# Optimization experiments

Hardware: AMD Instinct MI355X
Metric: run time of the kernel (lower is better)

Reference implementation:

```python
import jax, jax.numpy as jnp
import numpy as np

HOPS = 3  # C[i].weight tied to A[i+1].weight -> HOPS+1 distinct tables E_0..E_HOPS


def setup_inputs() -> dict:
    key = jax.random.key(0)
    ks = jax.random.split(key, 10)
    B, M, K, E, G, V = 32, 2048, 4, 128, 128, 50000
    s = 1.0 / np.sqrt(E).astype(np.float32)
    context = jax.random.randint(ks[0], (B, M, K), 0, V)          # memory (triples)
    h_ = jax.random.normal(ks[1], (B, G), dtype=jnp.float32)      # prev GRU hidden
    y_ = jax.random.randint(ks[2], (B,), 0, V)                    # prev token
    emb = jax.random.normal(ks[3], (HOPS + 1, V, E), dtype=jnp.float32) * 0.1
    W_ih = jax.random.normal(ks[4], (3 * G, E), dtype=jnp.float32) * s
    W_hh = jax.random.normal(ks[5], (3 * G, G), dtype=jnp.float32) * s
    b_ih = jax.random.normal(ks[6], (3 * G,), dtype=jnp.float32) * s
    b_hh = jax.random.normal(ks[7], (3 * G,), dtype=jnp.float32) * s
    W_vocab = jax.random.normal(ks[8], (V, 2 * E), dtype=jnp.float32) * s
    b_vocab = jax.random.normal(ks[9], (V,), dtype=jnp.float32) * s
    return dict(context=context, h_=h_, y_=y_, emb=emb, W_ih=W_ih, W_hh=W_hh,
                b_ih=b_ih, b_hh=b_hh, W_vocab=W_vocab, b_vocab=b_vocab)


def gru_cell(x, h, W_ih, W_hh, b_ih, b_hh):
    # PyTorch GRU cell semantics (r, z, n gate order).
    gi = x @ W_ih.T + b_ih
    gh = h @ W_hh.T + b_hh
    i_r, i_z, i_n = jnp.split(gi, 3, axis=-1)
    h_r, h_z, h_n = jnp.split(gh, 3, axis=-1)
    r = jax.nn.sigmoid(i_r + h_r)
    z = jax.nn.sigmoid(i_z + h_z)
    n = jnp.tanh(i_n + r * h_n)
    return (1.0 - z) * n + z * h


def reference(context, h_, y_, emb, W_ih, W_hh, b_ih, b_hh, W_vocab, b_vocab):
    x = emb[0][y_]                                   # [B, E] A[0] embed of prev token
    h = gru_cell(x, h_, W_ih, W_hh, b_ih, b_hh)      # [B, G], G == E
    q = h
    o1 = None
    attn = None
    for hop in range(HOPS):
        mA = emb[hop][context].sum(axis=2)           # gather [B,M,K,E] -> sum over K -> [B,M,E]
        p = jnp.einsum('bme,be->bm', mA, q)          # attention scores over memory slots
        attn = jax.nn.softmax(p, axis=1)             # [B, M]
        mC = emb[hop + 1][context].sum(axis=2)       # C[hop] table (tied to A[hop+1])
        o = jnp.einsum('bm,bme->be', attn, mC)       # memory read [B, E]
        q = q + o
        if hop == 0:
            o1 = o
    logits = jnp.concatenate([h, o1], axis=1) @ W_vocab.T + b_vocab  # [B, V]
    p_vocab = jax.nn.softmax(logits, axis=1)
    return h, p_vocab, attn
```

## Files before the change

### kernel.cpp

```cpp
#include <hip/hip_runtime.h>
#include <math.h>

#define BB 32
#define MM 2048
#define KK 4
#define EE 128
#define GG 128
#define VV 50000
#define HOPS 3

__global__ __launch_bounds__(384) void gru_kernel(
    const float* __restrict__ emb0,
    const int*   __restrict__ y,
    const float* __restrict__ hprev,
    const float* __restrict__ W_ih,
    const float* __restrict__ W_hh,
    const float* __restrict__ b_ih,
    const float* __restrict__ b_hh,
    float* __restrict__ h_out,
    float* __restrict__ q)
{
    int b = blockIdx.x;
    int t = threadIdx.x;
    __shared__ float x[EE], h[GG], gi[3*GG], gh[3*GG];
    if (t < EE)            x[t]       = emb0[(size_t)y[b]*EE + t];
    else if (t < 2*EE)     h[t-EE]    = hprev[b*GG + (t-EE)];
    __syncthreads();
    {
        float accI = b_ih[t], accH = b_hh[t];
        const float* wi = W_ih + (size_t)t*EE;
        const float* wh = W_hh + (size_t)t*GG;
        #pragma unroll 8
        for (int e = 0; e < EE; e++) { accI += x[e]*wi[e]; accH += h[e]*wh[e]; }
        gi[t] = accI; gh[t] = accH;
    }
    __syncthreads();
    if (t < GG) {
        float r = 1.f/(1.f + __expf(-(gi[t]        + gh[t])));
        float z = 1.f/(1.f + __expf(-(gi[GG+t]     + gh[GG+t])));
        float n = tanhf(gi[2*GG+t] + r*gh[2*GG+t]);
        float hn = (1.f - z)*n + z*h[t];
        h_out[b*GG + t] = hn;
        q[b*GG + t]     = hn;
    }
}

__global__ __launch_bounds__(256) void scores_kernel(
    const float* __restrict__ embT,
    const int*   __restrict__ ctx,
    const float* __restrict__ q,
    float* __restrict__ p)
{
    int gid  = blockIdx.x * 4 + (threadIdx.x >> 6);
    int lane = threadIdx.x & 63;
    int b    = gid >> 11;
    const int4 c = *(const int4*)(ctx + (size_t)gid*KK);
    float2 qv = *(const float2*)(q + b*EE + lane*2);
    float2 v0 = *(const float2*)(embT + (size_t)c.x*EE + lane*2);
    float2 v1 = *(const float2*)(embT + (size_t)c.y*EE + lane*2);
    float2 v2 = *(const float2*)(embT + (size_t)c.z*EE + lane*2);
    float2 v3 = *(const float2*)(embT + (size_t)c.w*EE + lane*2);
    float sx = v0.x + v1.x + v2.x + v3.x;
    float sy = v0.y + v1.y + v2.y + v3.y;
    float acc = sx*qv.x + sy*qv.y;
    #pragma unroll
    for (int off = 32; off; off >>= 1) acc += __shfl_down(acc, off);
    if (lane == 0) p[gid] = acc;
}

__global__ __launch_bounds__(256) void softmax_m_kernel(
    const float* __restrict__ p,
    float* __restrict__ attn)
{
    int b = blockIdx.x, t = threadIdx.x;
    const float* row = p + (size_t)b*MM;
    float v[8];
    float mx = -INFINITY;
    #pragma unroll
    for (int i = 0; i < 8; i++) { v[i] = row[t + i*256]; mx = fmaxf(mx, v[i]); }
    __shared__ float red[6];
    int w = t >> 6, lane = t & 63;
    #pragma unroll
    for (int off = 32; off; off >>= 1) mx = fmaxf(mx, __shfl_down(mx, off));
    if (lane == 0) red[w] = mx;
    __syncthreads();
    if (t == 0) { float m2 = fmaxf(fmaxf(red[0],red[1]), fmaxf(red[2],red[3])); red[4] = m2; }
    __syncthreads();
    mx = red[4];
    float sum = 0.f;
    #pragma unroll
    for (int i = 0; i < 8; i++) { v[i] = __expf(v[i] - mx); sum += v[i]; }
    #pragma unroll
    for (int off = 32; off; off >>= 1) sum += __shfl_down(sum, off);
    if (lane == 0) red[w] = sum;
    __syncthreads();
    if (t == 0) { red[5] = 1.f / (red[0]+red[1]+red[2]+red[3]); }
    __syncthreads();
    float rs = red[5];
    #pragma unroll
    for (int i = 0; i < 8; i++) attn[(size_t)b*MM + t + i*256] = v[i]*rs;
}

__global__ __launch_bounds__(256) void oacc_kernel(
    const float* __restrict__ embT,
    const int*   __restrict__ ctx,
    const float* __restrict__ attn,
    float* __restrict__ o_part)
{
    int blk = blockIdx.x;
    int b = blk >> 5, s = blk & 31;
    int w = threadIdx.x >> 6, lane = threadIdx.x & 63;
    int m0 = s*64 + w*16;
    float ax = 0.f, ay = 0.f;
    for (int i = 0; i < 16; i++) {
        int m = m0 + i;
        float a = attn[(size_t)b*MM + m];
        const int4 c = *(const int4*)(ctx + (size_t)(b*MM + m)*KK);
        float2 v0 = *(const float2*)(embT + (size_t)c.x*EE + lane*2);
        float2 v1 = *(const float2*)(embT + (size_t)c.y*EE + lane*2);
        float2 v2 = *(const float2*)(embT + (size_t)c.z*EE + lane*2);
        float2 v3 = *(const float2*)(embT + (size_t)c.w*EE + lane*2);
        ax += a * (v0.x + v1.x + v2.x + v3.x);
        ay += a * (v0.y + v1.y + v2.y + v3.y);
    }
    __shared__ float red[4][EE];
    red[w][lane*2]   = ax;
    red[w][lane*2+1] = ay;
    __syncthreads();
    if (threadIdx.x < EE) {
        int e = threadIdx.x;
        float v = red[0][e] + red[1][e] + red[2][e] + red[3][e];
        o_part[((size_t)s*BB + b)*EE + e] = v;
    }
}

__global__ __launch_bounds__(256) void qupd_kernel(
    const float* __restrict__ o_part,
    float* __restrict__ q,
    float* __restrict__ o1,
    int save_o1)
{
    int i = blockIdx.x*256 + threadIdx.x;
    float v = 0.f;
    #pragma unroll 8
    for (int s = 0; s < 32; s++) v += o_part[(size_t)s*BB*EE + i];
    q[i] += v;
    if (save_o1) o1[i] = v;
}

__global__ __launch_bounds__(256) void logits_kernel(
    const float* __restrict__ h,
    const float* __restrict__ o1,
    const float* __restrict__ Wv,
    const float* __restrict__ bv,
    float* __restrict__ logits)
{
    __shared__ float Ut[256][32];
    __shared__ float Wt[32][132];
    int t = threadIdx.x;
    for (int i = t; i < 256*32; i += 256) {
        int e = i >> 5, b = i & 31;
        Ut[e][b] = (e < GG) ? h[b*GG + e] : o1[b*EE + (e - GG)];
    }
    int vg = t & 31;
    int bg = t >> 5;
    int v0 = blockIdx.x * 128;
    float acc[4][4];
    #pragma unroll
    for (int i = 0; i < 4; i++)
        #pragma unroll
        for (int j = 0; j < 4; j++) acc[i][j] = 0.f;

    int vrow = t >> 1;
    int half = t & 1;
    const float* wrow = Wv + (size_t)(v0 + vrow)*256 + half*16;
    bool vok = (v0 + vrow) < VV;

    for (int ec = 0; ec < 256; ec += 32) {
        __syncthreads();
        #pragma unroll
        for (int j = 0; j < 4; j++) {
            float4 w = make_float4(0.f, 0.f, 0.f, 0.f);
            if (vok) w = *(const float4*)(wrow + ec + j*4);
            int e0 = half*16 + j*4;
            Wt[e0+0][vrow] = w.x;
            Wt[e0+1][vrow] = w.y;
            Wt[e0+2][vrow] = w.z;
            Wt[e0+3][vrow] = w.w;
        }
        __syncthreads();
        #pragma unroll 8
        for (int e = 0; e < 32; e++) {
            float4 w = *(const float4*)(&Wt[e][vg*4]);
            float4 u = *(const float4*)(&Ut[ec + e][bg*4]);
            acc[0][0] += w.x*u.x; acc[0][1] += w.x*u.y; acc[0][2] += w.x*u.z; acc[0][3] += w.x*u.w;
            acc[1][0] += w.y*u.x; acc[1][1] += w.y*u.y; acc[1][2] += w.y*u.z; acc[1][3] += w.y*u.w;
            acc[2][0] += w.z*u.x; acc[2][1] += w.z*u.y; acc[2][2] += w.z*u.z; acc[2][3] += w.z*u.w;
            acc[3][0] += w.w*u.x; acc[3][1] += w.w*u.y; acc[3][2] += w.w*u.z; acc[3][3] += w.w*u.w;
        }
    }
    #pragma unroll
    for (int i = 0; i < 4; i++) {
        int v = v0 + vg*4 + i;
        if (v < VV) {
            float bb = bv[v];
            #pragma unroll
            for (int j = 0; j < 4; j++)
                logits[(size_t)(bg*4 + j)*VV + v] = acc[i][j] + bb;
        }
    }
}

#define VCHUNK 6250
__global__ __launch_bounds__(256) void vpart_kernel(
    const float* __restrict__ logits,
    float* __restrict__ part)
{
    int blk = blockIdx.x;
    int b = blk >> 3, c = blk & 7;
    int t = threadIdx.x;
    const float* row = logits + (size_t)b*VV;
    int start = c*VCHUNK;
    int end   = min(start + VCHUNK, VV);
    __shared__ float red[4];
    int w = t >> 6, lane = t & 63;
    float mx = -INFINITY;
    for (int i = start + t; i < end; i += 256) mx = fmaxf(mx, row[i]);
    #pragma unroll
    for (int off = 32; off; off >>= 1) mx = fmaxf(mx, __shfl_down(mx, off));
    if (lane == 0) red[w] = mx;
    __syncthreads();
    float m = fmaxf(fmaxf(red[0], red[1]), fmaxf(red[2], red[3]));
    float sum = 0.f;
    for (int i = start + t; i < end; i += 256) sum += __expf(row[i] - m);
    #pragma unroll
    for (int off = 32; off; off >>= 1) sum += __shfl_down(sum, off);
    __syncthreads();
    if (lane == 0) red[w] = sum;
    __syncthreads();
    if (t == 0) {
        part[blk*2]   = m;
        part[blk*2+1] = red[0] + red[1] + red[2] + red[3];
    }
}

__global__ __launch_bounds__(256) void vfinal_kernel(
    float* __restrict__ logits,
    const float* __restrict__ part)
{
    int i = blockIdx.x*256 + threadIdx.x;
    if (i >= BB*VV) return;
    int b = i / VV;
    const float* pp = part + b*16;
    float M = -INFINITY;
    #pragma unroll
    for (int c = 0; c < 8; c++) M = fmaxf(M, pp[c*2]);
    float S = 0.f;
    #pragma unroll
    for (int c = 0; c < 8; c++) S += pp[c*2+1] * __expf(pp[c*2] - M);
    logits[i] = __expf(logits[i] - M) * (1.f / S);
}

extern "C" void kernel_launch(void* const* d_in, const int* in_sizes, int n_in,
                              void* d_out, int out_size, void* d_ws, size_t ws_size,
                              hipStream_t stream) {
    const int*   ctx    = (const int*)  d_in[0];
    const float* h_prev = (const float*)d_in[1];
    const int*   y      = (const int*)  d_in[2];
    const float* emb    = (const float*)d_in[3];
    const float* W_ih   = (const float*)d_in[4];
    const float* W_hh   = (const float*)d_in[5];
    const float* b_ih   = (const float*)d_in[6];
    const float* b_hh   = (const float*)d_in[7];
    const float* Wv     = (const float*)d_in[8];
    const float* bv     = (const float*)d_in[9];

    float* out_h    = (float*)d_out;
    float* out_pv   = out_h + BB*GG;
    float* out_attn = out_pv + (size_t)BB*VV;

    float* ws     = (float*)d_ws;
    float* q      = ws;
    float* o1     = q + BB*EE;
    float* o_part = o1 + BB*EE;
    float* p      = o_part + 32*BB*EE;
    float* attn   = p + BB*MM;
    float* part   = attn + BB*MM;

    gru_kernel<<<BB, 384, 0, stream>>>(emb, y, h_prev, W_ih, W_hh, b_ih, b_hh, out_h, q);

    for (int hop = 0; hop < HOPS; hop++) {
        const float* embA = emb + (size_t)hop*VV*EE;
        const float* embC = emb + (size_t)(hop+1)*VV*EE;
        scores_kernel<<<(BB*MM)/4, 256, 0, stream>>>(embA, ctx, q, p);
        float* attn_dst = (hop == HOPS-1) ? out_attn : attn;
        softmax_m_kernel<<<BB, 256, 0, stream>>>(p, attn_dst);
        oacc_kernel<<<BB*32, 256, 0, stream>>>(embC, ctx, attn_dst, o_part);
        qupd_kernel<<<(BB*EE)/256, 256, 0, stream>>>(o_part, q, o1, hop == 0 ? 1 : 0);
    }

    logits_kernel<<<(VV + 127)/128, 256, 0, stream>>>(out_h, o1, Wv, bv, out_pv);
    vpart_kernel<<<BB*8, 256, 0, stream>>>(out_pv, part);
    vfinal_kernel<<<(BB*VV + 255)/256, 256, 0, stream>>>(out_pv, part);
}
```

Baseline: 360.5 us.

## Replace per-slot embedding gathers with vocab-space dense GEMMs and scatter-add

Attention scores are computed as d = E_hop·q over the whole vocabulary using a tiled GEMM, then gathered per memory slot by summing four scalar lookups. The memory read scatters attention weights into a per-batch vocabulary histogram with atomics and multiplies it by the next embedding table in a dense tiled kernel. The final hop skips the unused read. This trades random gathers of 128-float rows for streaming the full 50000x128 tables per hop, plus atomics and larger workspaces, and it changes the floating-point summation order.

```diff
diff --git a/kernel.cpp b/kernel.cpp
--- a/kernel.cpp
+++ b/kernel.cpp
@@ -45,46 +45,89 @@
     }
 }
 
-__global__ __launch_bounds__(256) void scores_kernel(
-    const float* __restrict__ embT,
+__global__ __launch_bounds__(256) void dvec_kernel(
+    const float* __restrict__ q,
+    const float* __restrict__ W,
+    float* __restrict__ d)
+{
+    __shared__ float Ut[128][32];
+    __shared__ float Wt[32][132];
+    int t = threadIdx.x;
+    for (int i = t; i < 128*32; i += 256) {
+        int e = i >> 5, b = i & 31;
+        Ut[e][b] = q[b*EE + e];
+    }
+    int vg = t & 31;
+    int bg = t >> 5;
+    int v0 = blockIdx.x * 128;
+    float acc[4][4];
+    #pragma unroll
+    for (int i = 0; i < 4; i++)
+        #pragma unroll
+        for (int j = 0; j < 4; j++) acc[i][j] = 0.f;
+
+    int vrow = t >> 1;
+    int half = t & 1;
+    const float* wrow = W + (size_t)(v0 + vrow)*128 + half*16;
+    bool vok = (v0 + vrow) < VV;
+
+    for (int ec = 0; ec < 128; ec += 32) {
+        __syncthreads();
+        #pragma unroll
+        for (int j = 0; j < 4; j++) {
+            float4 w = make_float4(0.f, 0.f, 0.f, 0.f);
+            if (vok) w = *(const float4*)(wrow + ec + j*4);
+            int e0 = half*16 + j*4;
+            Wt[e0+0][vrow] = w.x;
+            Wt[e0+1][vrow] = w.y;
+            Wt[e0+2][vrow] = w.z;
+            Wt[e0+3][vrow] = w.w;
+        }
+        __syncthreads();
+        #pragma unroll 8
+        for (int e = 0; e < 32; e++) {
+            float4 w = *(const float4*)(&Wt[e][vg*4]);
+            float4 u = *(const float4*)(&Ut[ec + e][bg*4]);
+            acc[0][0] += w.x*u.x; acc[0][1] += w.x*u.y; acc[0][2] += w.x*u.z; acc[0][3] += w.x*u.w;
+            acc[1][0] += w.y*u.x; acc[1][1] += w.y*u.y; acc[1][2] += w.y*u.z; acc[1][3] += w.y*u.w;
+            acc[2][0] += w.z*u.x; acc[2][1] += w.z*u.y; acc[2][2] += w.z*u.z; acc[2][3] += w.z*u.w;
+            acc[3][0] += w.w*u.x; acc[3][1] += w.w*u.y; acc[3][2] += w.w*u.z; acc[3][3] += w.w*u.w;
+        }
+    }
+    #pragma unroll
+    for (int i = 0; i < 4; i++) {
+        int v = v0 + vg*4 + i;
+        if (v < VV) {
+            #pragma unroll
+            for (int j = 0; j < 4; j++)
+                d[(size_t)(bg*4 + j)*VV + v] = acc[i][j];
+        }
+    }
+}
+
+__global__ __launch_bounds__(256) void attn_kernel(
+    const float* __restrict__ d,
     const int*   __restrict__ ctx,
-    const float* __restrict__ q,
-    float* __restrict__ p)
-{
-    int gid  = blockIdx.x * 4 + (threadIdx.x >> 6);
-    int lane = threadIdx.x & 63;
-    int b    = gid >> 11;
-    const int4 c = *(const int4*)(ctx + (size_t)gid*KK);
-    float2 qv = *(const float2*)(q + b*EE + lane*2);
-    float2 v0 = *(const float2*)(embT + (size_t)c.x*EE + lane*2);
-    float2 v1 = *(const float2*)(embT + (size_t)c.y*EE + lane*2);
-    float2 v2 = *(const float2*)(embT + (size_t)c.z*EE + lane*2);
-    float2 v3 = *(const float2*)(embT + (size_t)c.w*EE + lane*2);
-    float sx = v0.x + v1.x + v2.x + v3.x;
-    float sy = v0.y + v1.y + v2.y + v3.y;
-    float acc = sx*qv.x + sy*qv.y;
-    #pragma unroll
-    for (int off = 32; off; off >>= 1) acc += __shfl_down(acc, off);
-    if (lane == 0) p[gid] = acc;
-}
-
-__global__ __launch_bounds__(256) void softmax_m_kernel(
-    const float* __restrict__ p,
     float* __restrict__ attn)
 {
     int b = blockIdx.x, t = threadIdx.x;
-    const float* row = p + (size_t)b*MM;
+    const float* db = d + (size_t)b*VV;
     float v[8];
     float mx = -INFINITY;
     #pragma unroll
-    for (int i = 0; i < 8; i++) { v[i] = row[t + i*256]; mx = fmaxf(mx, v[i]); }
+    for (int i = 0; i < 8; i++) {
+        int m = t + i*256;
+        const int4 c = *(const int4*)(ctx + (size_t)(b*MM + m)*KK);
+        v[i] = db[c.x] + db[c.y] + db[c.z] + db[c.w];
+        mx = fmaxf(mx, v[i]);
+    }
     __shared__ float red[6];
     int w = t >> 6, lane = t & 63;
     #pragma unroll
     for (int off = 32; off; off >>= 1) mx = fmaxf(mx, __shfl_down(mx, off));
     if (lane == 0) red[w] = mx;
     __syncthreads();
-    if (t == 0) { float m2 = fmaxf(fmaxf(red[0],red[1]), fmaxf(red[2],red[3])); red[4] = m2; }
+    if (t == 0) { red[4] = fmaxf(fmaxf(red[0],red[1]), fmaxf(red[2],red[3])); }
     __syncthreads();
     mx = red[4];
     float sum = 0.f;
@@ -101,36 +144,81 @@
     for (int i = 0; i < 8; i++) attn[(size_t)b*MM + t + i*256] = v[i]*rs;
 }
 
-__global__ __launch_bounds__(256) void oacc_kernel(
-    const float* __restrict__ embT,
+__global__ __launch_bounds__(256) void zero_kernel(float* __restrict__ w, int n4)
+{
+    int i = blockIdx.x*256 + threadIdx.x;
+    if (i < n4) ((float4*)w)[i] = make_float4(0.f,0.f,0.f,0.f);
+}
+
+__global__ __launch_bounds__(256) void scatter_kernel(
+    const float* __restrict__ attn,
     const int*   __restrict__ ctx,
-    const float* __restrict__ attn,
+    float* __restrict__ w)
+{
+    int gid = blockIdx.x*256 + threadIdx.x;
+    float a = attn[gid];
+    int b = gid >> 11;
+    const int4 c = *(const int4*)(ctx + (size_t)gid*KK);
+    float* wb = w + (size_t)b*VV;
+    atomicAdd(&wb[c.x], a);
+    atomicAdd(&wb[c.y], a);
+    atomicAdd(&wb[c.z], a);
+    atomicAdd(&wb[c.w], a);
+}
+
+#define OCH 196
+__global__ __launch_bounds__(256) void oaccv_kernel(
+    const float* __restrict__ emb,
+    const float* __restrict__ w,
     float* __restrict__ o_part)
 {
-    int blk = blockIdx.x;
-    int b = blk >> 5, s = blk & 31;
-    int w = threadIdx.x >> 6, lane = threadIdx.x & 63;
-    int m0 = s*64 + w*16;
-    float ax = 0.f, ay = 0.f;
-    for (int i = 0; i < 16; i++) {
-        int m = m0 + i;
-        float a = attn[(size_t)b*MM + m];
-        const int4 c = *(const int4*)(ctx + (size_t)(b*MM + m)*KK);
-        float2 v0 = *(const float2*)(embT + (size_t)c.x*EE + lane*2);
-        float2 v1 = *(const float2*)(embT + (size_t)c.y*EE + lane*2);
-        float2 v2 = *(const float2*)(embT + (size_t)c.z*EE + lane*2);
-        float2 v3 = *(const float2*)(embT + (size_t)c.w*EE + lane*2);
-        ax += a * (v0.x + v1.x + v2.x + v3.x);
-        ay += a * (v0.y + v1.y + v2.y + v3.y);
-    }
-    __shared__ float red[4][EE];
-    red[w][lane*2]   = ax;
-    red[w][lane*2+1] = ay;
-    __syncthreads();
-    if (threadIdx.x < EE) {
-        int e = threadIdx.x;
-        float v = red[0][e] + red[1][e] + red[2][e] + red[3][e];
-        o_part[((size_t)s*BB + b)*EE + e] = v;
+    __shared__ float embS[64][128];
+    __shared__ float wS[64][32];
+    int t = threadIdx.x;
+    int bg = t >> 6;
+    int eg = t & 63;
+    int v0 = blockIdx.x * OCH;
+    int vend = min(v0 + OCH, VV);
+    float acc[8][2];
+    #pragma unroll
+    for (int j = 0; j < 8; j++) { acc[j][0] = 0.f; acc[j][1] = 0.f; }
+
+    for (int vs = v0; vs < vend; vs += 64) {
+        int nv = vend - vs; if (nv > 64) nv = 64;
+        __syncthreads();
+        for (int i = t; i < 64*32; i += 256) {
+            int row = i >> 5, c4 = i & 31;
+            float4 val = make_float4(0.f,0.f,0.f,0.f);
+            if (row < nv) val = *(const float4*)(emb + (size_t)(vs+row)*128 + c4*4);
+            *(float4*)(&embS[row][c4*4]) = val;
+        }
+        for (int i = t; i < 512; i += 256) {
+            int b = i >> 4, vv = (i & 15)*4;
+            float4 val = make_float4(0.f,0.f,0.f,0.f);
+            if (vv < nv) val = *(const float4*)(w + (size_t)b*VV + vs + vv);
+            wS[vv+0][b] = val.x; wS[vv+1][b] = val.y;
+            wS[vv+2][b] = val.z; wS[vv+3][b] = val.w;
+        }
+        __syncthreads();
+        for (int vv = 0; vv < nv; vv++) {
+            float2 ev = *(const float2*)(&embS[vv][eg*2]);
+            float4 w0 = *(const float4*)(&wS[vv][bg*8]);
+            float4 w1 = *(const float4*)(&wS[vv][bg*8+4]);
+            acc[0][0] += w0.x*ev.x; acc[0][1] += w0.x*ev.y;
+            acc[1][0] += w0.y*ev.x; acc[1][1] += w0.y*ev.y;
+            acc[2][0] += w0.z*ev.x; acc[2][1] += w0.z*ev.y;
+            acc[3][0] += w0.w*ev.x; acc[3][1] += w0.w*ev.y;
+            acc[4][0] += w1.x*ev.x; acc[4][1] += w1.x*ev.y;
+            acc[5][0] += w1.y*ev.x; acc[5][1] += w1.y*ev.y;
+            acc[6][0] += w1.z*ev.x; acc[6][1] += w1.z*ev.y;
+            acc[7][0] += w1.w*ev.x; acc[7][1] += w1.w*ev.y;
+        }
+    }
+    float* op = o_part + (size_t)blockIdx.x*BB*EE;
+    #pragma unroll
+    for (int j = 0; j < 8; j++) {
+        op[(bg*8+j)*EE + eg*2]     = acc[j][0];
+        op[(bg*8+j)*EE + eg*2 + 1] = acc[j][1];
     }
 }
 
@@ -143,7 +231,7 @@
     int i = blockIdx.x*256 + threadIdx.x;
     float v = 0.f;
     #pragma unroll 8
-    for (int s = 0; s < 32; s++) v += o_part[(size_t)s*BB*EE + i];
+    for (int s = 0; s < 256; s++) v += o_part[(size_t)s*BB*EE + i];
     q[i] += v;
     if (save_o1) o1[i] = v;
 }
@@ -282,20 +370,27 @@
     float* ws     = (float*)d_ws;
     float* q      = ws;
     float* o1     = q + BB*EE;
-    float* o_part = o1 + BB*EE;
-    float* p      = o_part + 32*BB*EE;
-    float* attn   = p + BB*MM;
+    float* d      = o1 + BB*EE;
+    float* w      = d + (size_t)BB*VV;
+    float* o_part = w + (size_t)BB*VV;
+    float* attn   = o_part + 256*BB*EE;
     float* part   = attn + BB*MM;
+
+    const int dvec_grid = (VV + 127)/128;
+    const int w4 = (BB*VV)/4;
 
     gru_kernel<<<BB, 384, 0, stream>>>(emb, y, h_prev, W_ih, W_hh, b_ih, b_hh, out_h, q);
 
     for (int hop = 0; hop < HOPS; hop++) {
         const float* embA = emb + (size_t)hop*VV*EE;
+        dvec_kernel<<<dvec_grid, 256, 0, stream>>>(q, embA, d);
+        float* attn_dst = (hop == HOPS-1) ? out_attn : attn;
+        attn_kernel<<<BB, 256, 0, stream>>>(d, ctx, attn_dst);
+        if (hop == HOPS-1) break;
         const float* embC = emb + (size_t)(hop+1)*VV*EE;
-        scores_kernel<<<(BB*MM)/4, 256, 0, stream>>>(embA, ctx, q, p);
-        float* attn_dst = (hop == HOPS-1) ? out_attn : attn;
-        softmax_m_kernel<<<BB, 256, 0, stream>>>(p, attn_dst);
-        oacc_kernel<<<BB*32, 256, 0, stream>>>(embC, ctx, attn_dst, o_part);
+        zero_kernel<<<(w4 + 255)/256, 256, 0, stream>>>(w, w4);
+        scatter_kernel<<<(BB*MM)/256, 256, 0, stream>>>(attn_dst, ctx, w);
+        oaccv_kernel<<<256, 256, 0, stream>>>(embC, w, o_part);
         qupd_kernel<<<(BB*EE)/256, 256, 0, stream>>>(o_part, q, o1, hop == 0 ? 1 : 0);
     }
 
```

After: 423.9 us. 17.6% more time.

## Replace memory gathers with dense table-vector products and scattered attention weights

Applied to the files above, without the earlier changes.

The per-slot embedding gathers are replaced by linear algebra. Scores become a dense product of each embedding table with the query (d = E·q over all V), followed by a cheap scalar gather of d at the context indices. The memory read scatters the attention weights into a per-vocab weight vector with atomics and then does a dense streaming product with the C table. This turns random 512-byte row gathers into coalesced full-table streams, which means reading whole 25 MB tables several times per call. It also adds float atomics, which make the summation order nondeterministic. The logits GEMM is also retiled.

```diff
diff --git a/kernel.cpp b/kernel.cpp
--- a/kernel.cpp
+++ b/kernel.cpp
@@ -9,220 +9,266 @@
 #define VV 50000
 #define HOPS 3
 
-__global__ __launch_bounds__(384) void gru_kernel(
-    const float* __restrict__ emb0,
-    const int*   __restrict__ y,
+__global__ __launch_bounds__(256) void gru_zero_kernel(
+    const float* __restrict__ emb0, const int* __restrict__ y,
     const float* __restrict__ hprev,
-    const float* __restrict__ W_ih,
-    const float* __restrict__ W_hh,
-    const float* __restrict__ b_ih,
-    const float* __restrict__ b_hh,
-    float* __restrict__ h_out,
-    float* __restrict__ q)
-{
-    int b = blockIdx.x;
+    const float* __restrict__ W_ih, const float* __restrict__ W_hh,
+    const float* __restrict__ b_ih, const float* __restrict__ b_hh,
+    float* __restrict__ h_out, float* __restrict__ q0,
+    float* __restrict__ wz)
+{
+    int blk = blockIdx.x, t = threadIdx.x;
+    if (blk < BB) {
+        int b = blk;
+        __shared__ float x[EE], hh[GG], gi[3*GG], gh[3*GG];
+        if (t < EE)          x[t]     = emb0[(size_t)y[b]*EE + t];
+        else if (t < 2*EE)   hh[t-EE] = hprev[b*GG + (t-EE)];
+        __syncthreads();
+        for (int g = t; g < 3*GG; g += 256) {
+            float accI = b_ih[g], accH = b_hh[g];
+            const float* wi = W_ih + (size_t)g*EE;
+            const float* wh = W_hh + (size_t)g*GG;
+            #pragma unroll 8
+            for (int e = 0; e < EE; e++) { accI += x[e]*wi[e]; accH += hh[e]*wh[e]; }
+            gi[g] = accI; gh[g] = accH;
+        }
+        __syncthreads();
+        if (t < GG) {
+            float r = 1.f/(1.f + __expf(-(gi[t]      + gh[t])));
+            float z = 1.f/(1.f + __expf(-(gi[GG+t]   + gh[GG+t])));
+            float n = tanhf(gi[2*GG+t] + r*gh[2*GG+t]);
+            float hn = (1.f - z)*n + z*hh[t];
+            h_out[b*GG + t] = hn;
+            q0[b*GG + t]    = hn;
+        }
+    } else {
+        const int total4 = (2*BB*VV)/4;
+        float4* wp = (float4*)wz;
+        for (int i = (blk-BB)*256 + t; i < total4; i += 256*256)
+            wp[i] = make_float4(0.f,0.f,0.f,0.f);
+    }
+}
+
+__global__ __launch_bounds__(256) void dvec_kernel(
+    const float* __restrict__ q0, const float* __restrict__ oa0,
+    const float* __restrict__ oa1, int hop,
+    const float* __restrict__ W, float* __restrict__ d)
+{
+    __shared__ float q2[4096];
     int t = threadIdx.x;
-    __shared__ float x[EE], h[GG], gi[3*GG], gh[3*GG];
-    if (t < EE)            x[t]       = emb0[(size_t)y[b]*EE + t];
-    else if (t < 2*EE)     h[t-EE]    = hprev[b*GG + (t-EE)];
-    __syncthreads();
-    {
-        float accI = b_ih[t], accH = b_hh[t];
-        const float* wi = W_ih + (size_t)t*EE;
-        const float* wh = W_hh + (size_t)t*GG;
-        #pragma unroll 8
-        for (int e = 0; e < EE; e++) { accI += x[e]*wi[e]; accH += h[e]*wh[e]; }
-        gi[t] = accI; gh[t] = accH;
-    }
-    __syncthreads();
-    if (t < GG) {
-        float r = 1.f/(1.f + __expf(-(gi[t]        + gh[t])));
-        float z = 1.f/(1.f + __expf(-(gi[GG+t]     + gh[GG+t])));
-        float n = tanhf(gi[2*GG+t] + r*gh[2*GG+t]);
-        float hn = (1.f - z)*n + z*h[t];
-        h_out[b*GG + t] = hn;
-        q[b*GG + t]     = hn;
-    }
-}
-
-__global__ __launch_bounds__(256) void scores_kernel(
-    const float* __restrict__ embT,
-    const int*   __restrict__ ctx,
-    const float* __restrict__ q,
+    for (int i = t; i < 4096; i += 256) {
+        int e = i >> 5, b = i & 31;
+        float v = q0[b*EE + e];
+        if (hop >= 1) v += oa0[b*EE + e];
+        if (hop >= 2) v += oa1[b*EE + e];
+        q2[(e >> 2)*128 + b*4 + (e & 3)] = v;
+    }
+    __syncthreads();
+    int lane = t & 63, bg = t >> 6;
+    int v = blockIdx.x*64 + lane;
+    const float4* row = (const float4*)(W + (size_t)(v < VV ? v : VV-1)*EE);
+    float acc[8];
+    #pragma unroll
+    for (int k = 0; k < 8; k++) acc[k] = 0.f;
+    #pragma unroll 4
+    for (int c = 0; c < 32; c++) {
+        float4 wv = row[c];
+        const float4* uq = (const float4*)(q2 + c*128 + bg*32);
+        #pragma unroll
+        for (int k = 0; k < 8; k++) {
+            float4 u = uq[k];
+            acc[k] += wv.x*u.x + wv.y*u.y + wv.z*u.z + wv.w*u.w;
+        }
+    }
+    if (v < VV) {
+        #pragma unroll
+        for (int k = 0; k < 8; k++)
+            d[(size_t)(bg*8 + k)*VV + v] = acc[k];
+    }
+}
+
+__global__ __launch_bounds__(256) void pgather_kernel(
+    const float* __restrict__ d, const int* __restrict__ ctx,
     float* __restrict__ p)
 {
-    int gid  = blockIdx.x * 4 + (threadIdx.x >> 6);
-    int lane = threadIdx.x & 63;
-    int b    = gid >> 11;
+    int gid = blockIdx.x*256 + threadIdx.x;
+    int b = gid >> 11;
     const int4 c = *(const int4*)(ctx + (size_t)gid*KK);
-    float2 qv = *(const float2*)(q + b*EE + lane*2);
-    float2 v0 = *(const float2*)(embT + (size_t)c.x*EE + lane*2);
-    float2 v1 = *(const float2*)(embT + (size_t)c.y*EE + lane*2);
-    float2 v2 = *(const float2*)(embT + (size_t)c.z*EE + lane*2);
-    float2 v3 = *(const float2*)(embT + (size_t)c.w*EE + lane*2);
-    float sx = v0.x + v1.x + v2.x + v3.x;
-    float sy = v0.y + v1.y + v2.y + v3.y;
-    float acc = sx*qv.x + sy*qv.y;
-    #pragma unroll
-    for (int off = 32; off; off >>= 1) acc += __shfl_down(acc, off);
-    if (lane == 0) p[gid] = acc;
-}
-
-__global__ __launch_bounds__(256) void softmax_m_kernel(
-    const float* __restrict__ p,
-    float* __restrict__ attn)
+    const float* db = d + (size_t)b*VV;
+    p[gid] = db[c.x] + db[c.y] + db[c.z] + db[c.w];
+}
+
+__global__ __launch_bounds__(256) void softmax_sc_kernel(
+    const float* __restrict__ p, const int* __restrict__ ctx,
+    float* __restrict__ w,
+    float* __restrict__ out_attn,
+    int mode)
 {
     int b = blockIdx.x, t = threadIdx.x;
     const float* row = p + (size_t)b*MM;
-    float v[8];
+    float pv[8];
     float mx = -INFINITY;
     #pragma unroll
-    for (int i = 0; i < 8; i++) { v[i] = row[t + i*256]; mx = fmaxf(mx, v[i]); }
-    __shared__ float red[6];
-    int w = t >> 6, lane = t & 63;
+    for (int i = 0; i < 8; i++) { pv[i] = row[t + i*256]; mx = fmaxf(mx, pv[i]); }
+    __shared__ float red[16];
+    int wv = t >> 6, lane = t & 63;
     #pragma unroll
     for (int off = 32; off; off >>= 1) mx = fmaxf(mx, __shfl_down(mx, off));
-    if (lane == 0) red[w] = mx;
-    __syncthreads();
-    if (t == 0) { float m2 = fmaxf(fmaxf(red[0],red[1]), fmaxf(red[2],red[3])); red[4] = m2; }
+    if (lane == 0) red[wv] = mx;
+    __syncthreads();
+    if (t == 0) red[4] = fmaxf(fmaxf(red[0],red[1]), fmaxf(red[2],red[3]));
     __syncthreads();
     mx = red[4];
     float sum = 0.f;
     #pragma unroll
-    for (int i = 0; i < 8; i++) { v[i] = __expf(v[i] - mx); sum += v[i]; }
+    for (int i = 0; i < 8; i++) { pv[i] = __expf(pv[i] - mx); sum += pv[i]; }
     #pragma unroll
     for (int off = 32; off; off >>= 1) sum += __shfl_down(sum, off);
-    if (lane == 0) red[w] = sum;
-    __syncthreads();
-    if (t == 0) { red[5] = 1.f / (red[0]+red[1]+red[2]+red[3]); }
-    __syncthreads();
-    float rs = red[5];
-    #pragma unroll
-    for (int i = 0; i < 8; i++) attn[(size_t)b*MM + t + i*256] = v[i]*rs;
-}
-
-__global__ __launch_bounds__(256) void oacc_kernel(
-    const float* __restrict__ embT,
-    const int*   __restrict__ ctx,
-    const float* __restrict__ attn,
+    if (lane == 0) red[8 + wv] = sum;
+    __syncthreads();
+    if (t == 0) red[13] = 1.f / (red[8]+red[9]+red[10]+red[11]);
+    __syncthreads();
+    float rs = red[13];
+    if (mode) {
+        #pragma unroll
+        for (int i = 0; i < 8; i++)
+            out_attn[b*MM + t + i*256] = pv[i]*rs;
+    } else {
+        float* wb = w + (size_t)b*VV;
+        const int4* cb = (const int4*)ctx + b*MM;
+        #pragma unroll
+        for (int i = 0; i < 8; i++) {
+            float av = pv[i]*rs;
+            int4 c = cb[t + i*256];
+            atomicAdd(wb + c.x, av);
+            atomicAdd(wb + c.y, av);
+            atomicAdd(wb + c.z, av);
+            atomicAdd(wb + c.w, av);
+        }
+    }
+}
+
+#define OCH 98
+__global__ __launch_bounds__(256) void oaccv_kernel(
+    const float* __restrict__ emb, const float* __restrict__ w,
     float* __restrict__ o_part)
 {
-    int blk = blockIdx.x;
-    int b = blk >> 5, s = blk & 31;
-    int w = threadIdx.x >> 6, lane = threadIdx.x & 63;
-    int m0 = s*64 + w*16;
-    float ax = 0.f, ay = 0.f;
-    for (int i = 0; i < 16; i++) {
-        int m = m0 + i;
-        float a = attn[(size_t)b*MM + m];
-        const int4 c = *(const int4*)(ctx + (size_t)(b*MM + m)*KK);
-        float2 v0 = *(const float2*)(embT + (size_t)c.x*EE + lane*2);
-        float2 v1 = *(const float2*)(embT + (size_t)c.y*EE + lane*2);
-        float2 v2 = *(const float2*)(embT + (size_t)c.z*EE + lane*2);
-        float2 v3 = *(const float2*)(embT + (size_t)c.w*EE + lane*2);
-        ax += a * (v0.x + v1.x + v2.x + v3.x);
-        ay += a * (v0.y + v1.y + v2.y + v3.y);
-    }
-    __shared__ float red[4][EE];
-    red[w][lane*2]   = ax;
-    red[w][lane*2+1] = ay;
-    __syncthreads();
-    if (threadIdx.x < EE) {
-        int e = threadIdx.x;
-        float v = red[0][e] + red[1][e] + red[2][e] + red[3][e];
-        o_part[((size_t)s*BB + b)*EE + e] = v;
+    __shared__ float embS[64*128];
+    __shared__ float wS[64*32];
+    int t = threadIdx.x;
+    int bg = t >> 6, lane = t & 63;
+    int v0 = blockIdx.x * OCH;
+    int vend = min(v0 + OCH, VV);
+    float acc[8][2];
+    #pragma unroll
+    for (int j = 0; j < 8; j++) { acc[j][0] = 0.f; acc[j][1] = 0.f; }
+
+    for (int vs = v0; vs < vend; vs += 64) {
+        int nv = vend - vs; if (nv > 64) nv = 64;
+        __syncthreads();
+        for (int i = t; i < 64*32; i += 256) {
+            int rowi = i >> 5, c4 = i & 31;
+            float4 val = make_float4(0.f,0.f,0.f,0.f);
+            if (rowi < nv) val = *(const float4*)(emb + (size_t)(vs+rowi)*EE + c4*4);
+            *(float4*)(embS + rowi*128 + c4*4) = val;
+        }
+        for (int i = t; i < 512; i += 256) {
+            int b = i >> 4, vv4 = (i & 15)*4;
+            float4 val = make_float4(0.f,0.f,0.f,0.f);
+            if (vv4 < nv) val = *(const float4*)(w + (size_t)b*VV + vs + vv4);
+            wS[(vv4+0)*32 + b] = val.x;
+            wS[(vv4+1)*32 + b] = val.y;
+            wS[(vv4+2)*32 + b] = val.z;
+            wS[(vv4+3)*32 + b] = val.w;
+        }
+        __syncthreads();
+        for (int vv = 0; vv < nv; vv++) {
+            float2 ev  = *(const float2*)(embS + vv*128 + lane*2);
+            float4 w0v = *(const float4*)(wS + vv*32 + bg*8);
+            float4 w1v = *(const float4*)(wS + vv*32 + bg*8 + 4);
+            acc[0][0] += w0v.x*ev.x; acc[0][1] += w0v.x*ev.y;
+            acc[1][0] += w0v.y*ev.x; acc[1][1] += w0v.y*ev.y;
+            acc[2][0] += w0v.z*ev.x; acc[2][1] += w0v.z*ev.y;
+            acc[3][0] += w0v.w*ev.x; acc[3][1] += w0v.w*ev.y;
+            acc[4][0] += w1v.x*ev.x; acc[4][1] += w1v.x*ev.y;
+            acc[5][0] += w1v.y*ev.x; acc[5][1] += w1v.y*ev.y;
+            acc[6][0] += w1v.z*ev.x; acc[6][1] += w1v.z*ev.y;
+            acc[7][0] += w1v.w*ev.x; acc[7][1] += w1v.w*ev.y;
+        }
+    }
+    float* op = o_part + (size_t)blockIdx.x*BB*EE;
+    #pragma unroll
+    for (int j = 0; j < 8; j++) {
+        float2 r; r.x = acc[j][0]; r.y = acc[j][1];
+        *(float2*)(op + (bg*8+j)*EE + lane*2) = r;
     }
 }
 
 __global__ __launch_bounds__(256) void qupd_kernel(
     const float* __restrict__ o_part,
-    float* __restrict__ q,
-    float* __restrict__ o1,
-    int save_o1)
-{
-    int i = blockIdx.x*256 + threadIdx.x;
+    float* __restrict__ o_acc)
+{
+    int i0 = blockIdx.x * 64;
+    int sq = threadIdx.x >> 6;
+    int il = threadIdx.x & 63;
     float v = 0.f;
-    #pragma unroll 8
-    for (int s = 0; s < 32; s++) v += o_part[(size_t)s*BB*EE + i];
-    q[i] += v;
-    if (save_o1) o1[i] = v;
+    for (int s = sq; s < 512; s += 4)
+        v += o_part[(size_t)s*BB*EE + i0 + il];
+    __shared__ float red[4][64];
+    red[sq][il] = v;
+    __syncthreads();
+    if (threadIdx.x < 64)
+        o_acc[i0 + threadIdx.x] = red[0][threadIdx.x] + red[1][threadIdx.x]
+                                + red[2][threadIdx.x] + red[3][threadIdx.x];
 }
 
 __global__ __launch_bounds__(256) void logits_kernel(
-    const float* __restrict__ h,
-    const float* __restrict__ o1,
-    const float* __restrict__ Wv,
-    const float* __restrict__ bv,
+    const float* __restrict__ q0, const float* __restrict__ o1,
+    const float* __restrict__ Wv, const float* __restrict__ bv,
     float* __restrict__ logits)
 {
-    __shared__ float Ut[256][32];
-    __shared__ float Wt[32][132];
+    __shared__ float u2[8192];
     int t = threadIdx.x;
-    for (int i = t; i < 256*32; i += 256) {
+    for (int i = t; i < 8192; i += 256) {
         int e = i >> 5, b = i & 31;
-        Ut[e][b] = (e < GG) ? h[b*GG + e] : o1[b*EE + (e - GG)];
-    }
-    int vg = t & 31;
-    int bg = t >> 5;
-    int v0 = blockIdx.x * 128;
-    float acc[4][4];
-    #pragma unroll
-    for (int i = 0; i < 4; i++)
-        #pragma unroll
-        for (int j = 0; j < 4; j++) acc[i][j] = 0.f;
-
-    int vrow = t >> 1;
-    int half = t & 1;
-    const float* wrow = Wv + (size_t)(v0 + vrow)*256 + half*16;
-    bool vok = (v0 + vrow) < VV;
-
-    for (int ec = 0; ec < 256; ec += 32) {
-        __syncthreads();
-        #pragma unroll
-        for (int j = 0; j < 4; j++) {
-            float4 w = make_float4(0.f, 0.f, 0.f, 0.f);
-            if (vok) w = *(const float4*)(wrow + ec + j*4);
-            int e0 = half*16 + j*4;
-            Wt[e0+0][vrow] = w.x;
-            Wt[e0+1][vrow] = w.y;
-            Wt[e0+2][vrow] = w.z;
-            Wt[e0+3][vrow] = w.w;
-        }
-        __syncthreads();
-        #pragma unroll 8
-        for (int e = 0; e < 32; e++) {
-            float4 w = *(const float4*)(&Wt[e][vg*4]);
-            float4 u = *(const float4*)(&Ut[ec + e][bg*4]);
-            acc[0][0] += w.x*u.x; acc[0][1] += w.x*u.y; acc[0][2] += w.x*u.z; acc[0][3] += w.x*u.w;
-            acc[1][0] += w.y*u.x; acc[1][1] += w.y*u.y; acc[1][2] += w.y*u.z; acc[1][3] += w.y*u.w;
-            acc[2][0] += w.z*u.x; acc[2][1] += w.z*u.y; acc[2][2] += w.z*u.z; acc[2][3] += w.z*u.w;
-            acc[3][0] += w.w*u.x; acc[3][1] += w.w*u.y; acc[3][2] += w.w*u.z; acc[3][3] += w.w*u.w;
-        }
-    }
-    #pragma unroll
-    for (int i = 0; i < 4; i++) {
-        int v = v0 + vg*4 + i;
-        if (v < VV) {
-            float bb = bv[v];
-            #pragma unroll
-            for (int j = 0; j < 4; j++)
-                logits[(size_t)(bg*4 + j)*VV + v] = acc[i][j] + bb;
-        }
+        float v = (e < GG) ? q0[b*GG + e] : o1[b*EE + (e - GG)];
+        u2[(e >> 2)*128 + b*4 + (e & 3)] = v;
+    }
+    __syncthreads();
+    int lane = t & 63, bg = t >> 6;
+    int v = blockIdx.x*64 + lane;
+    const float4* row = (const float4*)(Wv + (size_t)(v < VV ? v : VV-1)*256);
+    float acc[8];
+    #pragma unroll
+    for (int k = 0; k < 8; k++) acc[k] = 0.f;
+    #pragma unroll 4
+    for (int c = 0; c < 64; c++) {
+        float4 wv = row[c];
+        const float4* uq = (const float4*)(u2 + c*128 + bg*32);
+        #pragma unroll
+        for (int k = 0; k < 8; k++) {
+            float4 u = uq[k];
+            acc[k] += wv.x*u.x + wv.y*u.y + wv.z*u.z + wv.w*u.w;
+        }
+    }
+    if (v < VV) {
+        float bb = bv[v];
+        #pragma unroll
+        for (int k = 0; k < 8; k++)
+            logits[(size_t)(bg*8 + k)*VV + v] = acc[k] + bb;
     }
 }
 
 #define VCHUNK 6250
 __global__ __launch_bounds__(256) void vpart_kernel(
-    const float* __restrict__ logits,
-    float* __restrict__ part)
+    const float* __restrict__ logits, float* __restrict__ part)
 {
     int blk = blockIdx.x;
     int b = blk >> 3, c = blk & 7;
     int t = threadIdx.x;
     const float* row = logits + (size_t)b*VV;
-    int start = c*VCHUNK;
-    int end   = min(start + VCHUNK, VV);
-    __shared__ float red[4];
+    int start = c*VCHUNK, end = min(start + VCHUNK, VV);
+    __shared__ float red[8];
     int w = t >> 6, lane = t & 63;
     float mx = -INFINITY;
     for (int i = start + t; i < end; i += 256) mx = fmaxf(mx, row[i]);
@@ -236,17 +282,16 @@
     #pragma unroll
     for (int off = 32; off; off >>= 1) sum += __shfl_down(sum, off);
     __syncthreads();
-    if (lane == 0) red[w] = sum;
+    if (lane == 0) red[4 + w] = sum;
     __syncthreads();
     if (t == 0) {
         part[blk*2]   = m;
-        part[blk*2+1] = red[0] + red[1] + red[2] + red[3];
+        part[blk*2+1] = red[4]+red[5]+red[6]+red[7];
     }
 }
 
 __global__ __launch_bounds__(256) void vfinal_kernel(
-    float* __restrict__ logits,
-    const float* __restrict__ part)
+    float* __restrict__ logits, const float* __restrict__ part)
 {
     int i = blockIdx.x*256 + threadIdx.x;
     if (i >= BB*VV) return;
@@ -280,26 +325,35 @@
     float* out_attn = out_pv + (size_t)BB*VV;
 
     float* ws     = (float*)d_ws;
-    float* q      = ws;
-    float* o1     = q + BB*EE;
-    float* o_part = o1 + BB*EE;
-    float* p      = o_part + 32*BB*EE;
-    float* attn   = p + BB*MM;
-    float* part   = attn + BB*MM;
-
-    gru_kernel<<<BB, 384, 0, stream>>>(emb, y, h_prev, W_ih, W_hh, b_ih, b_hh, out_h, q);
+    float* q0     = ws;
+    float* oa0    = q0 + BB*EE;
+    float* oa1    = oa0 + BB*EE;
+    float* part   = oa1 + BB*EE;
+    float* p      = part + 512;
+    float* dbuf   = p + BB*MM;
+    float* w0     = dbuf + (size_t)BB*VV;
+    float* w1     = w0 + (size_t)BB*VV;
+    float* o_part = w1 + (size_t)BB*VV;
+
+    const int row_grid = (VV + 63)/64;
+
+    gru_zero_kernel<<<BB + 256, 256, 0, stream>>>(emb, y, h_prev, W_ih, W_hh,
+                                                  b_ih, b_hh, out_h, q0, w0);
 
     for (int hop = 0; hop < HOPS; hop++) {
         const float* embA = emb + (size_t)hop*VV*EE;
+        int last = (hop == HOPS-1);
+        dvec_kernel<<<row_grid, 256, 0, stream>>>(q0, oa0, oa1, hop, embA, dbuf);
+        pgather_kernel<<<(BB*MM)/256, 256, 0, stream>>>(dbuf, ctx, p);
+        float* wdst = (hop == 0) ? w0 : w1;
+        softmax_sc_kernel<<<BB, 256, 0, stream>>>(p, ctx, wdst, out_attn, last);
+        if (last) break;
         const float* embC = emb + (size_t)(hop+1)*VV*EE;
-        scores_kernel<<<(BB*MM)/4, 256, 0, stream>>>(embA, ctx, q, p);
-        float* attn_dst = (hop == HOPS-1) ? out_attn : attn;
-        softmax_m_kernel<<<BB, 256, 0, stream>>>(p, attn_dst);
-        oacc_kernel<<<BB*32, 256, 0, stream>>>(embC, ctx, attn_dst, o_part);
-        qupd_kernel<<<(BB*EE)/256, 256, 0, stream>>>(o_part, q, o1, hop == 0 ? 1 : 0);
-    }
-
-    logits_kernel<<<(VV + 127)/128, 256, 0, stream>>>(out_h, o1, Wv, bv, out_pv);
+        oaccv_kernel<<<512, 256, 0, stream>>>(embC, wdst, o_part);
+        qupd_kernel<<<(BB*EE)/64, 256, 0, stream>>>(o_part, hop == 0 ? oa0 : oa1);
+    }
+
+    logits_kernel<<<row_grid, 256, 0, stream>>>(q0, oa0, Wv, bv, out_pv);
     vpart_kernel<<<BB*8, 256, 0, stream>>>(out_pv, part);
     vfinal_kernel<<<(BB*VV + 255)/256, 256, 0, stream>>>(out_pv, part);
 }
```

Result: slower. 500.9 us (+38.9%).
